# Optimization experiments

Hardware: AMD Instinct MI355X
Metric: run time of the kernel (lower is better)

The kernel has to match this reference:

```python
import jax, jax.numpy as jnp
import numpy as np

DIM = 512
HEADS = 16
HEAD_DIM = DIM // HEADS
SCALE = HEAD_DIM ** -0.5


def setup_inputs() -> dict:
    key = jax.random.key(0)
    k = jax.random.split(key, 6)
    B_, N = 2048, 49
    nW = 64
    x = jax.random.normal(k[0], (B_, N, DIM), dtype=jnp.float32)
    mask = jax.random.normal(k[1], (nW, N, N), dtype=jnp.float32)
    W_qkv = jax.random.normal(k[2], (3 * DIM, DIM), dtype=jnp.float32) * 0.02
    b_qkv = jnp.zeros((3 * DIM,), dtype=jnp.float32)
    W_proj = jax.random.normal(k[3], (DIM, DIM), dtype=jnp.float32) * 0.02
    b_proj = jnp.zeros((DIM,), dtype=jnp.float32)
    return {"x": x, "mask": mask, "W_qkv": W_qkv, "b_qkv": b_qkv,
            "W_proj": W_proj, "b_proj": b_proj}


def reference(x, mask, W_qkv, b_qkv, W_proj, b_proj):
    B_, N, C = x.shape
    H, d = HEADS, HEAD_DIM
    nW = mask.shape[0]
    # qkv projection: [B_, N, 3, H, d] -> q,k,v each [B_, H, N, d]
    qkv = (x @ W_qkv.T + b_qkv).reshape(B_, N, 3, H, d)
    qkv = jnp.transpose(qkv, (2, 0, 3, 1, 4))
    q, k, v = qkv[0], qkv[1], qkv[2]
    attn = jnp.einsum('bhnd,bhmd->bhnm', q * SCALE, k)  # [B_, H, N, N]
    # add per-window additive mask, broadcast over B_//nW groups and heads
    attn = attn.reshape(B_ // nW, nW, H, N, N) + mask[None, :, None, :, :]
    attn = attn.reshape(B_, H, N, N)
    attn = jax.nn.softmax(attn, axis=-1)
    out = jnp.einsum('bhnm,bhmd->bhnd', attn, v)  # [B_, H, N, d]
    out = jnp.transpose(out, (0, 2, 1, 3)).reshape(B_, N, C)
    return out @ W_proj.T + b_proj
```

## Files before the change

### kernel.cpp

```cpp
#include <hip/hip_runtime.h>


typedef unsigned short ushort_t;
typedef __bf16 bf16x8 __attribute__((ext_vector_type(8)));
typedef float f32x4 __attribute__((ext_vector_type(4)));
typedef unsigned short us8 __attribute__((ext_vector_type(8)));

#define SCALE_F 0.17677669529663687f
constexpr size_t QKV_REG = 2048ULL * 16 * 49 * 32;

__device__ __forceinline__ ushort_t f2bf(float f) {
  unsigned u = __builtin_bit_cast(unsigned, f);
  u += 0x7FFFu + ((u >> 16) & 1u);
  return (ushort_t)(u >> 16);
}

__device__ __forceinline__ void gload_lds16(const void* g, void* l) {
  __builtin_amdgcn_global_load_lds(
      (const __attribute__((address_space(1))) void*)g,
      (__attribute__((address_space(3))) void*)l, 16, 0, 0);
}

__global__ __launch_bounds__(256) void k_cvt(const float* __restrict__ in,
                                             ushort_t* __restrict__ out, int n4) {
  int i = blockIdx.x * blockDim.x + threadIdx.x;
  if (i >= n4) return;
  float4 v = reinterpret_cast<const float4*>(in)[i];
  ushort4 o = make_ushort4(f2bf(v.x), f2bf(v.y), f2bf(v.z), f2bf(v.w));
  reinterpret_cast<ushort4*>(out)[i] = o;
}

template <int EPI>
__global__ __launch_bounds__(256) void k_gemm(const ushort_t* __restrict__ A,
                                              const ushort_t* __restrict__ W,
                                              const float* __restrict__ bias,
                                              ushort_t* __restrict__ out_qkv,
                                              float* __restrict__ out_f,
                                              int nt_o) {
  __shared__ __align__(16) ushort_t As[128][64];
  __shared__ __align__(16) ushort_t Ws[128][64];

  const int tid  = threadIdx.x;
  const int lane = tid & 63;
  const int wv   = tid >> 6;
  const int wr   = wv >> 1, wc = wv & 1;

  const int cpx = gridDim.x >> 3;
  const int lid = (blockIdx.x & 7) * cpx + (blockIdx.x >> 3);
  const int bm  = lid / nt_o;
  const int bo  = lid - bm * nt_o;
  const size_t m0 = (size_t)bm * 128;
  const int o0    = bo * 128;

  f32x4 acc[4][4];
#pragma unroll
  for (int i = 0; i < 4; i++)
#pragma unroll
    for (int j = 0; j < 4; j++) acc[i][j] = f32x4{0.f, 0.f, 0.f, 0.f};

  const int srow   = wv * 32 + (lane >> 3);
  const int schunk = (((lane & 7) ^ (lane >> 3)) * 8);

  for (int kt = 0; kt < 8; ++kt) {
    const int k0 = kt * 64;
#pragma unroll
    for (int i = 0; i < 4; i++)
      gload_lds16(A + (m0 + srow + i * 8) * 512 + k0 + schunk,
                  &As[wv * 32 + i * 8][0]);
#pragma unroll
    for (int i = 0; i < 4; i++)
      gload_lds16(W + (size_t)(o0 + srow + i * 8) * 512 + k0 + schunk,
                  &Ws[wv * 32 + i * 8][0]);
    __syncthreads();
    const int fr = lane & 15;
#pragma unroll
    for (int kk = 0; kk < 2; ++kk) {
      const int ch = kk * 4 + (lane >> 4);
      const int cb = ((ch ^ (lane & 7)) << 3);
      uint4 ar[4], br[4];
#pragma unroll
      for (int mi = 0; mi < 4; mi++)
        ar[mi] = *reinterpret_cast<const uint4*>(&As[wr * 64 + mi * 16 + fr][cb]);
#pragma unroll
      for (int ni = 0; ni < 4; ni++)
        br[ni] = *reinterpret_cast<const uint4*>(&Ws[wc * 64 + ni * 16 + fr][cb]);
#pragma unroll
      for (int mi = 0; mi < 4; mi++)
#pragma unroll
        for (int ni = 0; ni < 4; ni++)
          acc[mi][ni] = __builtin_amdgcn_mfma_f32_16x16x32_bf16(
              __builtin_bit_cast(bf16x8, ar[mi]),
              __builtin_bit_cast(bf16x8, br[ni]), acc[mi][ni], 0, 0, 0);
    }
    __syncthreads();
  }

  const int colbase = lane & 15;
  const int rowgrp  = (lane >> 4) * 4;

  if constexpr (EPI == 1) {
#pragma unroll
    for (int ni = 0; ni < 4; ni++) {
      const int o = o0 + wc * 64 + ni * 16 + colbase;
      const float bv = bias[o];
#pragma unroll
      for (int mi = 0; mi < 4; mi++) {
        const size_t mrow = m0 + wr * 64 + mi * 16 + rowgrp;
#pragma unroll
        for (int r = 0; r < 4; r++)
          out_f[(mrow + r) * 512 + o] = acc[mi][ni][r] + bv;
      }
    }
  } else {
#pragma unroll
    for (int mi = 0; mi < 4; mi++) {
#pragma unroll
      for (int r = 0; r < 4; r++) {
        const int t = (int)m0 + wr * 64 + mi * 16 + rowgrp + r;
        const int b = t / 49;
        const int n = t - b * 49;
#pragma unroll
        for (int ni = 0; ni < 4; ni++) {
          const int o = o0 + wc * 64 + ni * 16 + colbase;
          const int which = o >> 9;
          const int h = (o >> 5) & 15;
          const int dd = o & 31;
          const size_t dst = (size_t)which * QKV_REG +
                             (((size_t)b * 16 + h) * 49 + n) * 32 + dd;
          out_qkv[dst] = f2bf(acc[mi][ni][r] + bias[o]);
        }
      }
    }
  }
}

__global__ __launch_bounds__(256) void k_attn4(const ushort_t* __restrict__ qkv,
                                               const float* __restrict__ mask,
                                               ushort_t* __restrict__ aout) {
  __shared__ __align__(16) ushort_t Vt[4][32][64];
  __shared__ __align__(16) ushort_t Ps[4][64][64];

  const int tid  = threadIdx.x;
  const int lane = tid & 63;
  const int wv   = tid >> 6;
  const int blk  = blockIdx.x;
  const int b    = blk >> 2;
  const int h    = (blk & 3) * 4 + wv;
  const int w    = b & 63;
  const size_t base = (((size_t)b * 16 + h)) * (49 * 32);
  const ushort_t* qb = qkv + base;
  const ushort_t* kb = qkv + QKV_REG + base;
  const ushort_t* vb = qkv + 2 * QKV_REG + base;

  {
    uint4* vz = reinterpret_cast<uint4*>(&Vt[wv][0][0]);
#pragma unroll
    for (int i = 0; i < 4; i++) vz[i * 64 + lane] = make_uint4(0, 0, 0, 0);
  }
  __syncthreads();
#pragma unroll
  for (int i = 0; i < 4; i++) {
    const int e = lane + (i << 6);
    if (e < 196) {
      const int n = e >> 2, d0 = (e & 3) * 8;
      uint4 raw = *reinterpret_cast<const uint4*>(vb + n * 32 + d0);
      us8 ev = __builtin_bit_cast(us8, raw);
#pragma unroll
      for (int j = 0; j < 8; j++)
        Vt[wv][d0 + j][(((n >> 3) ^ j) << 3) | (n & 7)] = ev[j];
    }
  }

  const int arow = lane & 15;
  const int kc   = (lane >> 4) * 8;
  const int rg   = (lane >> 4) * 4;

  uint4 kf[4];
#pragma unroll
  for (int ni = 0; ni < 4; ni++)
    kf[ni] = *reinterpret_cast<const uint4*>(kb + (ni * 16 + arow) * 32 + kc);

  float rsum[4][4];

#pragma unroll
  for (int hm = 0; hm < 2; hm++) {
    f32x4 s2[2][4];
#pragma unroll
    for (int j = 0; j < 2; j++) {
      const int mt = hm * 2 + j;
      uint4 qraw = *reinterpret_cast<const uint4*>(qb + (mt * 16 + arow) * 32 + kc);
      bf16x8 qa = __builtin_bit_cast(bf16x8, qraw);
#pragma unroll
      for (int ni = 0; ni < 4; ni++) {
        f32x4 z = {0.f, 0.f, 0.f, 0.f};
        s2[j][ni] = __builtin_amdgcn_mfma_f32_16x16x32_bf16(
            qa, __builtin_bit_cast(bf16x8, kf[ni]), z, 0, 0, 0);
      }
    }
#pragma unroll
    for (int j = 0; j < 2; j++) {
      const int mt = hm * 2 + j;
#pragma unroll
      for (int r = 0; r < 4; r++) {
        const int qr = mt * 16 + rg + r;
        float sv[4];
        float mx = -1e30f;
#pragma unroll
        for (int ni = 0; ni < 4; ni++) {
          const int col = ni * 16 + arow;
          float v;
          if (qr < 49 && col < 49)
            v = s2[j][ni][r] * SCALE_F + mask[(size_t)w * 2401 + qr * 49 + col];
          else
            v = -1e30f;
          sv[ni] = v;
          mx = fmaxf(mx, v);
        }
#pragma unroll
        for (int off = 1; off < 16; off <<= 1) mx = fmaxf(mx, __shfl_xor(mx, off));
        float sum = 0.f;
        const int prow = rg + r;
#pragma unroll
        for (int ni = 0; ni < 4; ni++) {
          float p = __expf(sv[ni] - mx);
          sum += p;
          const int pcol = ni * 16 + arow;
          Ps[wv][mt * 16 + prow]
            [(((pcol >> 3) ^ (prow & 7)) << 3) | (pcol & 7)] = f2bf(p);
        }
#pragma unroll
        for (int off = 1; off < 16; off <<= 1) sum += __shfl_xor(sum, off);
        rsum[mt][r] = sum;
      }
    }
  }

  __syncthreads();

  uint4 vf0[2], vf1[2];
#pragma unroll
  for (int kk = 0; kk < 2; kk++) {
    const int ch = kk * 4 + (lane >> 4);
    const int cb = ((ch ^ (lane & 7)) << 3);
    vf0[kk] = *reinterpret_cast<const uint4*>(&Vt[wv][arow][cb]);
    vf1[kk] = *reinterpret_cast<const uint4*>(&Vt[wv][16 + arow][cb]);
  }

#pragma unroll
  for (int mt = 0; mt < 4; mt++) {
    f32x4 o0 = {0.f, 0.f, 0.f, 0.f}, o1 = {0.f, 0.f, 0.f, 0.f};
#pragma unroll
    for (int kk = 0; kk < 2; kk++) {
      const int ch = kk * 4 + (lane >> 4);
      const int cb = ((ch ^ (lane & 7)) << 3);
      uint4 praw = *reinterpret_cast<const uint4*>(&Ps[wv][mt * 16 + arow][cb]);
      bf16x8 pa = __builtin_bit_cast(bf16x8, praw);
      o0 = __builtin_amdgcn_mfma_f32_16x16x32_bf16(
          pa, __builtin_bit_cast(bf16x8, vf0[kk]), o0, 0, 0, 0);
      o1 = __builtin_amdgcn_mfma_f32_16x16x32_bf16(
          pa, __builtin_bit_cast(bf16x8, vf1[kk]), o1, 0, 0, 0);
    }
#pragma unroll
    for (int r = 0; r < 4; r++) {
      const int qr = mt * 16 + rg + r;
      if (qr < 49) {
        const float inv = 1.f / rsum[mt][r];
        aout[((size_t)b * 49 + qr) * 512 + h * 32 + arow]      = f2bf(o0[r] * inv);
        aout[((size_t)b * 49 + qr) * 512 + h * 32 + 16 + arow] = f2bf(o1[r] * inv);
      }
    }
  }
}

extern "C" void kernel_launch(void* const* d_in, const int* in_sizes, int n_in,
                              void* d_out, int out_size, void* d_ws, size_t ws_size,
                              hipStream_t stream) {
  const float* x      = (const float*)d_in[0];
  const float* mask   = (const float*)d_in[1];
  const float* W_qkv  = (const float*)d_in[2];
  const float* b_qkv  = (const float*)d_in[3];
  const float* W_proj = (const float*)d_in[4];
  const float* b_proj = (const float*)d_in[5];
  float* out = (float*)d_out;

  ushort_t* ws     = (ushort_t*)d_ws;
  ushort_t* xb     = ws;
  ushort_t* qkvb   = ws + 51380224UL;
  ushort_t* aoutb  = ws + 205520896UL;
  ushort_t* wqkvb  = ws + 256901120UL;
  ushort_t* wprojb = ws + 257687552UL;

  const int n4x = 51380224 / 4, n4q = 786432 / 4, n4p = 262144 / 4;
  k_cvt<<<(n4x + 255) / 256, 256, 0, stream>>>(x, xb, n4x);
  k_cvt<<<(n4q + 255) / 256, 256, 0, stream>>>(W_qkv, wqkvb, n4q);
  k_cvt<<<(n4p + 255) / 256, 256, 0, stream>>>(W_proj, wprojb, n4p);

  k_gemm<0><<<784 * 12, 256, 0, stream>>>(xb, wqkvb, b_qkv, qkvb, nullptr, 12);

  k_attn4<<<2048 * 4, 256, 0, stream>>>(qkvb, mask, aoutb);

  k_gemm<1><<<784 * 4, 256, 0, stream>>>(aoutb, wprojb, b_proj, nullptr, out, 4);
}
```

Baseline: 574.7 us.

## Fuse fp32-to-bf16 conversion of x into QKV GEMM and store QKV row-major

Removes the separate conversion pass over x by loading fp32 tiles of x into shared memory and converting to bf16 inside the QKV GEMM. The QKV output is now written in natural token-major [token][1536] layout instead of a scattered per-head layout, and the attention kernel reads q/k/v with a strided row pitch. This cuts a full read/write pass over the activation but doubles global and shared-memory traffic for the A operand in the GEMM, and makes attention loads more strided.

```diff
diff --git a/kernel.cpp b/kernel.cpp
--- a/kernel.cpp
+++ b/kernel.cpp
@@ -7,7 +7,6 @@
 typedef unsigned short us8 __attribute__((ext_vector_type(8)));
 
 #define SCALE_F 0.17677669529663687f
-constexpr size_t QKV_REG = 2048ULL * 16 * 49 * 32;
 
 __device__ __forceinline__ ushort_t f2bf(float f) {
   unsigned u = __builtin_bit_cast(unsigned, f);
@@ -30,15 +29,13 @@
   reinterpret_cast<ushort4*>(out)[i] = o;
 }
 
-template <int EPI>
-__global__ __launch_bounds__(256) void k_gemm(const ushort_t* __restrict__ A,
-                                              const ushort_t* __restrict__ W,
-                                              const float* __restrict__ bias,
-                                              ushort_t* __restrict__ out_qkv,
-                                              float* __restrict__ out_f,
-                                              int nt_o) {
-  __shared__ __align__(16) ushort_t As[128][64];
+__global__ __launch_bounds__(256) void k_gemm1f(const float* __restrict__ X,
+                                                const ushort_t* __restrict__ W,
+                                                const float* __restrict__ bias,
+                                                ushort_t* __restrict__ out_qkv) {
+  __shared__ __align__(16) float    Asf[128][64];
   __shared__ __align__(16) ushort_t Ws[128][64];
+  constexpr int nt_o = 12;
 
   const int tid  = threadIdx.x;
   const int lane = tid & 63;
@@ -58,6 +55,103 @@
 #pragma unroll
     for (int j = 0; j < 4; j++) acc[i][j] = f32x4{0.f, 0.f, 0.f, 0.f};
 
+  const int l15 = lane & 15;
+  const int lq  = lane >> 4;
+  int schA[4];
+#pragma unroll
+  for (int i = 0; i < 4; i++)
+    schA[i] = (l15 ^ ((i * 4 + lq) & 15)) * 4;
+
+  const int srowW = wv * 32 + (lane >> 3);
+  const int schW  = ((lane & 7) ^ (lane >> 3)) * 8;
+  const ushort_t* Wg = W + (size_t)(o0 + srowW) * 512 + schW;
+
+  for (int kt = 0; kt < 8; ++kt) {
+    const int k0 = kt * 64;
+#pragma unroll
+    for (int i = 0; i < 8; i++) {
+      const float* g = X + (m0 + wv * 32 + i * 4 + lq) * 512 + k0 + schA[i & 3];
+      gload_lds16(g, &Asf[wv * 32 + i * 4][0]);
+    }
+#pragma unroll
+    for (int i = 0; i < 4; i++)
+      gload_lds16(Wg + (size_t)i * (8 * 512) + k0, &Ws[wv * 32 + i * 8][0]);
+    __syncthreads();
+
+    const int fr = lane & 15;
+#pragma unroll
+    for (int kk = 0; kk < 2; ++kk) {
+      const int cbW = (((kk * 4 + lq) ^ (lane & 7)) << 3);
+      uint4 br[4];
+#pragma unroll
+      for (int ni = 0; ni < 4; ni++)
+        br[ni] = *reinterpret_cast<const uint4*>(&Ws[wc * 64 + ni * 16 + fr][cbW]);
+      bf16x8 ar[4];
+      const int L0 = kk * 8 + lq * 2;
+      const int s0 = (L0 ^ fr) * 4;
+      const int s1 = ((L0 + 1) ^ fr) * 4;
+#pragma unroll
+      for (int mi = 0; mi < 4; mi++) {
+        const float4 fa = *reinterpret_cast<const float4*>(&Asf[wr * 64 + mi * 16 + fr][s0]);
+        const float4 fb = *reinterpret_cast<const float4*>(&Asf[wr * 64 + mi * 16 + fr][s1]);
+        bf16x8 t;
+        t[0] = (__bf16)fa.x; t[1] = (__bf16)fa.y; t[2] = (__bf16)fa.z; t[3] = (__bf16)fa.w;
+        t[4] = (__bf16)fb.x; t[5] = (__bf16)fb.y; t[6] = (__bf16)fb.z; t[7] = (__bf16)fb.w;
+        ar[mi] = t;
+      }
+#pragma unroll
+      for (int mi = 0; mi < 4; mi++)
+#pragma unroll
+        for (int ni = 0; ni < 4; ni++)
+          acc[mi][ni] = __builtin_amdgcn_mfma_f32_16x16x32_bf16(
+              ar[mi], __builtin_bit_cast(bf16x8, br[ni]), acc[mi][ni], 0, 0, 0);
+    }
+    __syncthreads();
+  }
+
+  const int colbase = lane & 15;
+  const int rowgrp  = (lane >> 4) * 4;
+#pragma unroll
+  for (int mi = 0; mi < 4; mi++) {
+#pragma unroll
+    for (int r = 0; r < 4; r++) {
+      const size_t t = m0 + wr * 64 + mi * 16 + rowgrp + r;
+      ushort_t* rowp = out_qkv + t * 1536;
+#pragma unroll
+      for (int ni = 0; ni < 4; ni++) {
+        const int o = o0 + wc * 64 + ni * 16 + colbase;
+        rowp[o] = f2bf(acc[mi][ni][r] + bias[o]);
+      }
+    }
+  }
+}
+
+__global__ __launch_bounds__(256) void k_gemmB(const ushort_t* __restrict__ A,
+                                               const ushort_t* __restrict__ W,
+                                               const float* __restrict__ bias,
+                                               float* __restrict__ out_f,
+                                               int nt_o) {
+  __shared__ __align__(16) ushort_t As[128][64];
+  __shared__ __align__(16) ushort_t Ws[128][64];
+
+  const int tid  = threadIdx.x;
+  const int lane = tid & 63;
+  const int wv   = tid >> 6;
+  const int wr   = wv >> 1, wc = wv & 1;
+
+  const int cpx = gridDim.x >> 3;
+  const int lid = (blockIdx.x & 7) * cpx + (blockIdx.x >> 3);
+  const int bm  = lid / nt_o;
+  const int bo  = lid - bm * nt_o;
+  const size_t m0 = (size_t)bm * 128;
+  const int o0    = bo * 128;
+
+  f32x4 acc[4][4];
+#pragma unroll
+  for (int i = 0; i < 4; i++)
+#pragma unroll
+    for (int j = 0; j < 4; j++) acc[i][j] = f32x4{0.f, 0.f, 0.f, 0.f};
+
   const int srow   = wv * 32 + (lane >> 3);
   const int schunk = (((lane & 7) ^ (lane >> 3)) * 8);
 
@@ -97,39 +191,16 @@
 
   const int colbase = lane & 15;
   const int rowgrp  = (lane >> 4) * 4;
-
-  if constexpr (EPI == 1) {
-#pragma unroll
-    for (int ni = 0; ni < 4; ni++) {
-      const int o = o0 + wc * 64 + ni * 16 + colbase;
-      const float bv = bias[o];
-#pragma unroll
-      for (int mi = 0; mi < 4; mi++) {
-        const size_t mrow = m0 + wr * 64 + mi * 16 + rowgrp;
-#pragma unroll
-        for (int r = 0; r < 4; r++)
-          out_f[(mrow + r) * 512 + o] = acc[mi][ni][r] + bv;
-      }
-    }
-  } else {
+#pragma unroll
+  for (int ni = 0; ni < 4; ni++) {
+    const int o = o0 + wc * 64 + ni * 16 + colbase;
+    const float bv = bias[o];
 #pragma unroll
     for (int mi = 0; mi < 4; mi++) {
-#pragma unroll
-      for (int r = 0; r < 4; r++) {
-        const int t = (int)m0 + wr * 64 + mi * 16 + rowgrp + r;
-        const int b = t / 49;
-        const int n = t - b * 49;
-#pragma unroll
-        for (int ni = 0; ni < 4; ni++) {
-          const int o = o0 + wc * 64 + ni * 16 + colbase;
-          const int which = o >> 9;
-          const int h = (o >> 5) & 15;
-          const int dd = o & 31;
-          const size_t dst = (size_t)which * QKV_REG +
-                             (((size_t)b * 16 + h) * 49 + n) * 32 + dd;
-          out_qkv[dst] = f2bf(acc[mi][ni][r] + bias[o]);
-        }
-      }
+      const size_t mrow = m0 + wr * 64 + mi * 16 + rowgrp;
+#pragma unroll
+      for (int r = 0; r < 4; r++)
+        out_f[(mrow + r) * 512 + o] = acc[mi][ni][r] + bv;
     }
   }
 }
@@ -147,10 +218,10 @@
   const int b    = blk >> 2;
   const int h    = (blk & 3) * 4 + wv;
   const int w    = b & 63;
-  const size_t base = (((size_t)b * 16 + h)) * (49 * 32);
-  const ushort_t* qb = qkv + base;
-  const ushort_t* kb = qkv + QKV_REG + base;
-  const ushort_t* vb = qkv + 2 * QKV_REG + base;
+  const size_t tb = (size_t)b * 49 * 1536 + (size_t)h * 32;
+  const ushort_t* qb = qkv + tb;
+  const ushort_t* kb = qkv + tb + 512;
+  const ushort_t* vb = qkv + tb + 1024;
 
   {
     uint4* vz = reinterpret_cast<uint4*>(&Vt[wv][0][0]);
@@ -163,7 +234,7 @@
     const int e = lane + (i << 6);
     if (e < 196) {
       const int n = e >> 2, d0 = (e & 3) * 8;
-      uint4 raw = *reinterpret_cast<const uint4*>(vb + n * 32 + d0);
+      uint4 raw = *reinterpret_cast<const uint4*>(vb + (size_t)n * 1536 + d0);
       us8 ev = __builtin_bit_cast(us8, raw);
 #pragma unroll
       for (int j = 0; j < 8; j++)
@@ -178,7 +249,7 @@
   uint4 kf[4];
 #pragma unroll
   for (int ni = 0; ni < 4; ni++)
-    kf[ni] = *reinterpret_cast<const uint4*>(kb + (ni * 16 + arow) * 32 + kc);
+    kf[ni] = *reinterpret_cast<const uint4*>(kb + (size_t)(ni * 16 + arow) * 1536 + kc);
 
   float rsum[4][4];
 
@@ -188,7 +259,7 @@
 #pragma unroll
     for (int j = 0; j < 2; j++) {
       const int mt = hm * 2 + j;
-      uint4 qraw = *reinterpret_cast<const uint4*>(qb + (mt * 16 + arow) * 32 + kc);
+      uint4 qraw = *reinterpret_cast<const uint4*>(qb + (size_t)(mt * 16 + arow) * 1536 + kc);
       bf16x8 qa = __builtin_bit_cast(bf16x8, qraw);
 #pragma unroll
       for (int ni = 0; ni < 4; ni++) {
@@ -284,20 +355,18 @@
   float* out = (float*)d_out;
 
   ushort_t* ws     = (ushort_t*)d_ws;
-  ushort_t* xb     = ws;
-  ushort_t* qkvb   = ws + 51380224UL;
-  ushort_t* aoutb  = ws + 205520896UL;
-  ushort_t* wqkvb  = ws + 256901120UL;
-  ushort_t* wprojb = ws + 257687552UL;
-
-  const int n4x = 51380224 / 4, n4q = 786432 / 4, n4p = 262144 / 4;
-  k_cvt<<<(n4x + 255) / 256, 256, 0, stream>>>(x, xb, n4x);
+  ushort_t* qkvb   = ws;
+  ushort_t* aoutb  = ws + 154140672UL;
+  ushort_t* wqkvb  = ws + 205520896UL;
+  ushort_t* wprojb = ws + 206307328UL;
+
+  const int n4q = 786432 / 4, n4p = 262144 / 4;
   k_cvt<<<(n4q + 255) / 256, 256, 0, stream>>>(W_qkv, wqkvb, n4q);
   k_cvt<<<(n4p + 255) / 256, 256, 0, stream>>>(W_proj, wprojb, n4p);
 
-  k_gemm<0><<<784 * 12, 256, 0, stream>>>(xb, wqkvb, b_qkv, qkvb, nullptr, 12);
+  k_gemm1f<<<784 * 12, 256, 0, stream>>>(x, wqkvb, b_qkv, qkvb);
 
   k_attn4<<<2048 * 4, 256, 0, stream>>>(qkvb, mask, aoutb);
 
-  k_gemm<1><<<784 * 4, 256, 0, stream>>>(aoutb, wprojb, b_proj, nullptr, out, 4);
-}
+  k_gemmB<<<784 * 4, 256, 0, stream>>>(aoutb, wprojb, b_proj, out, 4);
+}
```

After: 599.7 us. 4.3% more time.
